# Kernel tuning notes

Measured on AMD Instinct MI355X. Metric: run time of the kernel, lower is better.

Reference implementation:

```python
import jax, jax.numpy as jnp
import numpy as np

B, S, DM = 4, 2048, 512
H, D = 8, 64          # att_head, head_dim = att_dim // att_head
LEFT, RIGHT = 128, 128  # band_part(left_mask, right_mask)
LARGE = 1e30          # masked_softmax large number for fp32


def setup_inputs() -> dict:
    key = jax.random.key(0)
    ks = jax.random.split(key, 11)
    scale = 1.0 / np.sqrt(DM)
    x = jax.random.normal(ks[0], (B, S, DM), jnp.float32)
    Wq = jax.random.normal(ks[1], (DM, DM), jnp.float32) * scale
    bq = jnp.zeros((DM,), jnp.float32)
    Wk = jax.random.normal(ks[2], (DM, DM), jnp.float32) * scale
    bk = jnp.zeros((DM,), jnp.float32)
    Wv = jax.random.normal(ks[3], (DM, DM), jnp.float32) * scale
    bv = jnp.zeros((DM,), jnp.float32)
    Wo = jax.random.normal(ks[4], (DM, DM), jnp.float32) * scale
    bo = jnp.zeros((DM,), jnp.float32)
    x_len = jax.random.randint(ks[5], (B,), 0, 2048)
    return {"x": x, "Wq": Wq, "bq": bq, "Wk": Wk, "bk": bk,
            "Wv": Wv, "bv": bv, "Wo": Wo, "bo": bo, "x_len": x_len}


def reference(x, Wq, bq, Wk, bk, Wv, bv, Wo, bo, x_len):
    b, s, _ = x.shape
    # QKV projections, split into heads: [B,S,H,D]
    q = (x @ Wq + bq).reshape(b, s, H, D)
    k = (x @ Wk + bk).reshape(b, s, H, D)
    v = (x @ Wv + bv).reshape(b, s, H, D)
    # content energy: [B,H,Q,K], scaled by sqrt(head_dim)
    energy = jnp.einsum('bind,bjnd->bnij', q, k) / jnp.sqrt(jnp.float32(D))
    # banded mask (tf.linalg.band_part semantics): keep -LEFT <= j-i <= RIGHT
    i = jnp.arange(s)[:, None]
    j = jnp.arange(s)[None, :]
    band = ((j - i) <= RIGHT) & ((i - j) <= LEFT)            # [S,S]
    # key-length mask (tf.sequence_mask, expanded to [B,1,1,S])
    seq = jnp.arange(s)[None, :] < x_len[:, None]            # [B,S]
    mask = (band[None, None, :, :] & seq[:, None, None, :]).astype(energy.dtype)
    # masked softmax: energy - (1 - mask) * LARGE, softmax over keys
    att = jax.nn.softmax(energy - (1.0 - mask) * LARGE, axis=-1)
    # context: [B,Q,H,D] -> [B,S,H*D]
    ctx = jnp.einsum('bnij,bjnd->bind', att, v).reshape(b, s, H * D)
    # output projection (use_proj=True)
    return ctx @ Wo + bo
```

## Files before the change

### kernel.cpp

```cpp
#include <hip/hip_runtime.h>

#define S_LEN 2048
#define BATCH 4
#define DMODEL 512
#define NHEAD 8
#define HDIM 64
#define ROWS (BATCH * S_LEN)

using short8 = __attribute__((ext_vector_type(8))) short;
using f32x4  = __attribute__((ext_vector_type(4))) float;

__device__ __forceinline__ unsigned short f2bf(float f) {
  unsigned int u = __builtin_bit_cast(unsigned int, f);
  u += 0x7fffu + ((u >> 16) & 1u);
  return (unsigned short)(u >> 16);
}
__device__ __forceinline__ float bf2f(unsigned short h) {
  unsigned int u = ((unsigned int)h) << 16;
  return __builtin_bit_cast(float, u);
}
__device__ __forceinline__ void glds16(const void* g, void* l) {
  __builtin_amdgcn_global_load_lds((const __attribute__((address_space(1))) unsigned*)g,
                                   (__attribute__((address_space(3))) unsigned*)l, 16, 0, 0);
}

__global__ __launch_bounds__(256) void prep_kernel(const float* __restrict__ x,
                                                   const float* __restrict__ Wq,
                                                   const float* __restrict__ Wk,
                                                   const float* __restrict__ Wv,
                                                   const float* __restrict__ Wo,
                                                   unsigned short* __restrict__ xb,
                                                   unsigned short* __restrict__ WqkT,
                                                   unsigned short* __restrict__ WvT,
                                                   unsigned short* __restrict__ WoT) {
  __shared__ float t[32][33];
  const int blk = blockIdx.x, tid = threadIdx.x;
  if (blk < 2048) {
    const int base = (blk * 256 + tid) * 8;
    float4 f0 = *(const float4*)(x + base);
    float4 f1 = *(const float4*)(x + base + 4);
    uint4 o;
    o.x = (unsigned)f2bf(f0.x) | ((unsigned)f2bf(f0.y) << 16);
    o.y = (unsigned)f2bf(f0.z) | ((unsigned)f2bf(f0.w) << 16);
    o.z = (unsigned)f2bf(f1.x) | ((unsigned)f2bf(f1.y) << 16);
    o.w = (unsigned)f2bf(f1.z) | ((unsigned)f2bf(f1.w) << 16);
    *(uint4*)(xb + base) = o;
    return;
  }
  const int tb = blk - 2048;
  const int which = tb >> 8;
  const int tile = tb & 255;
  const float* W = which == 0 ? Wq : which == 1 ? Wk : which == 2 ? Wv : Wo;
  unsigned short* WT = which == 0 ? WqkT : which == 1 ? (WqkT + 512 * 512)
                      : which == 2 ? WvT : WoT;
  const int tx = tid & 31, ty = tid >> 5;
  const int x0 = (tile & 15) * 32, y0 = (tile >> 4) * 32;
#pragma unroll
  for (int r = 0; r < 4; r++)
    t[ty + 8 * r][tx] = W[(size_t)(y0 + ty + 8 * r) * DMODEL + x0 + tx];
  __syncthreads();
#pragma unroll
  for (int r = 0; r < 4; r++)
    WT[(size_t)(x0 + ty + 8 * r) * DMODEL + y0 + tx] = f2bf(t[tx][ty + 8 * r]);
}

__global__ __launch_bounds__(256, 2) void gemm_qkv_kernel(const unsigned short* __restrict__ xb,
                                                          const unsigned short* __restrict__ WqkT,
                                                          const unsigned short* __restrict__ WvT,
                                                          const float* __restrict__ bq,
                                                          const float* __restrict__ bk,
                                                          const float* __restrict__ bv,
                                                          const int* __restrict__ x_len,
                                                          unsigned short* __restrict__ Qb,
                                                          unsigned short* __restrict__ Kb,
                                                          unsigned short* __restrict__ Vt) {
  constexpr int K = DMODEL;
  __shared__ __align__(16) char smem[16384];
  char* As = smem;
  char* Bs = smem + 8192;
  const int bid = blockIdx.x;
  const bool vmode = bid < 256;
  const unsigned short *A, *Bt;
  int m0, n0;
  if (vmode) {
    m0 = (bid & 3) * 128;
    n0 = (bid >> 2) * 128;
    A = WvT; Bt = xb;
  } else {
    const int q = bid - 256;
    m0 = (q >> 3) * 128;
    n0 = (q & 7) * 128;
    A = xb; Bt = WqkT;
    const int xl = x_len[m0 >> 11];
    const int s0 = m0 & 2047;
    if (n0 >= DMODEL) { if (s0 >= xl) return; }
    else if (s0 >= xl + 128) return;
  }
  const int tid = threadIdx.x;
  const int wave = tid >> 6, lane = tid & 63;
  const int wr = wave >> 1, wc = wave & 1;
  const int lm = lane & 15, lq = lane >> 4;
  const int lr = lane >> 2;
  const int lc = (lane & 3) ^ ((lane >> 3) & 3);
  const unsigned short* gA0 = A + (size_t)(m0 + wave * 16 + lr) * K + lc * 8;
  const unsigned short* gA1 = A + (size_t)(m0 + (wave + 4) * 16 + lr) * K + lc * 8;
  const unsigned short* gB0 = Bt + (size_t)(n0 + wave * 16 + lr) * K + lc * 8;
  const unsigned short* gB1 = Bt + (size_t)(n0 + (wave + 4) * 16 + lr) * K + lc * 8;
  char* lA0 = As + wave * 1024 + lane * 16;
  char* lA1 = As + (wave + 4) * 1024 + lane * 16;
  char* lB0 = Bs + wave * 1024 + lane * 16;
  char* lB1 = Bs + (wave + 4) * 1024 + lane * 16;
  const int sw = (lm >> 1) & 3;
  int aoff[4], boff[4];
#pragma unroll
  for (int mi = 0; mi < 4; mi++)
    aoff[mi] = (wr * 64 + mi * 16 + lm) * 64 + (lq ^ sw) * 16;
#pragma unroll
  for (int ni = 0; ni < 4; ni++)
    boff[ni] = (wc * 64 + ni * 16 + lm) * 64 + (lq ^ sw) * 16;

  f32x4 acc[4][4] = {};
  for (int k0 = 0; k0 < K; k0 += 32) {
    __syncthreads();
    glds16(gA0 + k0, lA0);
    glds16(gA1 + k0, lA1);
    glds16(gB0 + k0, lB0);
    glds16(gB1 + k0, lB1);
    __syncthreads();
    short8 af[4], bfr[4];
#pragma unroll
    for (int mi = 0; mi < 4; mi++) af[mi] = *(const short8*)(As + aoff[mi]);
#pragma unroll
    for (int ni = 0; ni < 4; ni++) bfr[ni] = *(const short8*)(Bs + boff[ni]);
#pragma unroll
    for (int mi = 0; mi < 4; mi++)
#pragma unroll
      for (int ni = 0; ni < 4; ni++)
        acc[mi][ni] = __builtin_amdgcn_mfma_f32_16x16x32_bf16(af[mi], bfr[ni], acc[mi][ni], 0, 0, 0);
  }
#pragma unroll
  for (int mi = 0; mi < 4; mi++) {
    const int row0 = m0 + wr * 64 + mi * 16 + lq * 4;
#pragma unroll
    for (int ni = 0; ni < 4; ni++) {
      const int col = n0 + wc * 64 + ni * 16 + lm;
#pragma unroll
      for (int r = 0; r < 4; r++) {
        const int row = row0 + r;
        const float v = acc[mi][ni][r];
        if (vmode) {
          Vt[(size_t)row * ROWS + col] = f2bf(v + bv[row]);
        } else if (col < DMODEL) {
          Qb[(size_t)row * DMODEL + col] = f2bf(v + bq[col]);
        } else {
          Kb[(size_t)row * DMODEL + (col - DMODEL)] = f2bf(v + bk[col - DMODEL]);
        }
      }
    }
  }
}

__global__ __launch_bounds__(256) void vsum_kernel(const unsigned short* __restrict__ Vt,
                                                   float* __restrict__ vs) {
  const int wid = blockIdx.x * 4 + (threadIdx.x >> 6);
  const int lane = threadIdx.x & 63;
  const int b = wid >> 9, n = wid & 511;
  const unsigned short* row = Vt + (size_t)n * ROWS + b * S_LEN;
  float s = 0.f;
#pragma unroll
  for (int it = 0; it < 4; it++) {
    uint4 v = *(const uint4*)(row + it * 512 + lane * 8);
    unsigned int w[4] = {v.x, v.y, v.z, v.w};
#pragma unroll
    for (int e = 0; e < 4; e++) {
      s += bf2f((unsigned short)(w[e] & 0xffffu));
      s += bf2f((unsigned short)(w[e] >> 16));
    }
  }
#pragma unroll
  for (int off = 1; off < 64; off <<= 1) s += __shfl_xor(s, off, 64);
  if (lane == 0) vs[(size_t)b * DMODEL + n] = s;
}

__global__ __launch_bounds__(256) void tailrow_kernel(const float* __restrict__ vsum,
                                                      const unsigned short* __restrict__ WoT,
                                                      const float* __restrict__ bo,
                                                      float* __restrict__ trow) {
  const int b = blockIdx.y;
  const int wave = threadIdx.x >> 6, lane = threadIdx.x & 63;
  const float* vs = vsum + b * DMODEL + lane * 8;
  float vreg[8];
  *(float4*)vreg = *(const float4*)vs;
  *(float4*)(vreg + 4) = *(const float4*)(vs + 4);
#pragma unroll
  for (int ci = 0; ci < 8; ci++) {
    const int c = blockIdx.x * 32 + wave * 8 + ci;
    const uint4 wv = *(const uint4*)(WoT + (size_t)c * DMODEL + lane * 8);
    const unsigned int w[4] = {wv.x, wv.y, wv.z, wv.w};
    float acc = 0.f;
#pragma unroll
    for (int e = 0; e < 4; e++) {
      acc += vreg[2 * e] * bf2f((unsigned short)(w[e] & 0xffffu));
      acc += vreg[2 * e + 1] * bf2f((unsigned short)(w[e] >> 16));
    }
#pragma unroll
    for (int off = 1; off < 64; off <<= 1) acc += __shfl_xor(acc, off, 64);
    if (lane == 0) trow[b * DMODEL + c] = bo[c] + acc * (1.f / 2048.f);
  }
}

__global__ __launch_bounds__(256) void attn_kernel(const unsigned short* __restrict__ Q,
                                                   const unsigned short* __restrict__ K,
                                                   const unsigned short* __restrict__ Vt,
                                                   const int* __restrict__ x_len,
                                                   const float* __restrict__ vsum,
                                                   unsigned short* __restrict__ ctx) {
  __shared__ unsigned short Ks[32][72];
  __shared__ unsigned short Vs[64][40];
  __shared__ unsigned short Ps[4][16][40];
  const int tid = threadIdx.x;
  const int wave = tid >> 6, lane = tid & 63;
  const int lm = lane & 15, lq = lane >> 4;
  const int b = blockIdx.z, h = blockIdx.y;
  const int i0 = blockIdx.x * 64;
  const int q0 = i0 + wave * 16;
  const int xlen = x_len[b];
  const int t0 = min(S_LEN, xlen + 128);
  if ((i0 & ~127) >= t0) return;

  const size_t qoff = (size_t)(b * S_LEN + q0 + lm) * DMODEL + h * HDIM + lq * 8;
  const short8 aq0 = *(const short8*)(Q + qoff);
  const short8 aq1 = *(const short8*)(Q + qoff + 32);

  const int krow = tid >> 3, kchk = (tid & 7) * 8;
  const int vdim = tid >> 2, vchk = (tid & 3) * 8;

  f32x4 oacc[4] = {};
  float lrow[4] = {0.f, 0.f, 0.f, 0.f};

  for (int kt = 0; kt < 10; kt++) {
    const int jt0 = i0 - 128 + kt * 32;
    if (jt0 + 31 < 0 || jt0 >= xlen) continue;
    __syncthreads();
    {
      const int jr = jt0 + krow;
      const int jrc = min(max(jr, 0), S_LEN - 1);
      *(uint4*)&Ks[krow][kchk] =
          *(const uint4*)(K + (size_t)(b * S_LEN + jrc) * DMODEL + h * HDIM + kchk);
      const int jv = jt0 + vchk;
      const int jvc = min(max(jv, 0), S_LEN - 8);
      *(uint4*)&Vs[vdim][vchk] =
          *(const uint4*)(Vt + (size_t)(h * HDIM + vdim) * ROWS + b * S_LEN + jvc);
    }
    __syncthreads();
    if (jt0 + 31 < q0 - 128 || jt0 > q0 + 143) continue;

    f32x4 sv[2];
#pragma unroll
    for (int sub = 0; sub < 2; sub++) {
      const short8 bk0 = *(const short8*)&Ks[sub * 16 + lm][lq * 8];
      const short8 bk1 = *(const short8*)&Ks[sub * 16 + lm][32 + lq * 8];
      f32x4 s = {};
      s = __builtin_amdgcn_mfma_f32_16x16x32_bf16(aq0, bk0, s, 0, 0, 0);
      s = __builtin_amdgcn_mfma_f32_16x16x32_bf16(aq1, bk1, s, 0, 0, 0);
      sv[sub] = s;
    }
    float p[2][4];
#pragma unroll
    for (int sub = 0; sub < 2; sub++) {
      const int j = jt0 + sub * 16 + lm;
      const bool jv = (j >= 0) && (j < xlen);
#pragma unroll
      for (int r = 0; r < 4; r++) {
        const int i = q0 + lq * 4 + r;
        const bool ok = jv && (j - i <= 128) && (i - j <= 128);
        const float pv = ok ? __expf(sv[sub][r] * 0.125f) : 0.f;
        p[sub][r] = pv;
        lrow[r] += pv;
      }
    }
#pragma unroll
    for (int r = 0; r < 4; r++) {
      Ps[wave][lq * 4 + r][lm] = f2bf(p[0][r]);
      Ps[wave][lq * 4 + r][16 + lm] = f2bf(p[1][r]);
    }
    const short8 pf = *(const short8*)&Ps[wave][lm][lq * 8];
#pragma unroll
    for (int dt = 0; dt < 4; dt++) {
      const short8 bv = *(const short8*)&Vs[dt * 16 + lm][lq * 8];
      oacc[dt] = __builtin_amdgcn_mfma_f32_16x16x32_bf16(pf, bv, oacc[dt], 0, 0, 0);
    }
  }
#pragma unroll
  for (int r = 0; r < 4; r++)
#pragma unroll
    for (int off = 1; off < 16; off <<= 1) lrow[r] += __shfl_xor(lrow[r], off, 64);

#pragma unroll
  for (int r = 0; r < 4; r++) {
    const int i = q0 + lq * 4 + r;
    const size_t obase = (size_t)(b * S_LEN + i) * DMODEL + h * HDIM;
    if (lrow[r] > 0.f) {
      const float inv = 1.f / lrow[r];
#pragma unroll
      for (int dt = 0; dt < 4; dt++)
        ctx[obase + dt * 16 + lm] = f2bf(oacc[dt][r] * inv);
    } else {
#pragma unroll
      for (int dt = 0; dt < 4; dt++)
        ctx[obase + dt * 16 + lm] =
            f2bf(vsum[(size_t)b * DMODEL + h * HDIM + dt * 16 + lm] * (1.f / 2048.f));
    }
  }
}

__global__ __launch_bounds__(256, 2) void gemm_out_kernel(const unsigned short* __restrict__ A,
                                                          const unsigned short* __restrict__ Bt,
                                                          const float* __restrict__ bias,
                                                          const int* __restrict__ x_len,
                                                          const float* __restrict__ trow,
                                                          float* __restrict__ out) {
  constexpr int K = DMODEL;
  __shared__ __align__(16) char smem[16384];
  char* As = smem;
  char* Bs = smem + 8192;
  const int tid = threadIdx.x;
  const int m0 = blockIdx.y * 128, n0 = blockIdx.x * 128;
  {
    const int xl = x_len[m0 >> 11];
    if ((m0 & 2047) >= min(S_LEN, xl + 128)) {
      const float4 val = *(const float4*)(trow + (m0 >> 11) * DMODEL + n0 + (tid & 31) * 4);
      float* obase = out + (size_t)m0 * DMODEL + n0 + (tid & 31) * 4;
#pragma unroll
      for (int r = tid >> 5; r < 128; r += 8)
        *(float4*)(obase + (size_t)r * DMODEL) = val;
      return;
    }
  }
  const int wave = tid >> 6, lane = tid & 63;
  const int wr = wave >> 1, wc = wave & 1;
  const int lm = lane & 15, lq = lane >> 4;
  const int lr = lane >> 2;
  const int lc = (lane & 3) ^ ((lane >> 3) & 3);
  const unsigned short* gA0 = A + (size_t)(m0 + wave * 16 + lr) * K + lc * 8;
  const unsigned short* gA1 = A + (size_t)(m0 + (wave + 4) * 16 + lr) * K + lc * 8;
  const unsigned short* gB0 = Bt + (size_t)(n0 + wave * 16 + lr) * K + lc * 8;
  const unsigned short* gB1 = Bt + (size_t)(n0 + (wave + 4) * 16 + lr) * K + lc * 8;
  char* lA0 = As + wave * 1024 + lane * 16;
  char* lA1 = As + (wave + 4) * 1024 + lane * 16;
  char* lB0 = Bs + wave * 1024 + lane * 16;
  char* lB1 = Bs + (wave + 4) * 1024 + lane * 16;
  const int sw = (lm >> 1) & 3;
  int aoff[4], boff[4];
#pragma unroll
  for (int mi = 0; mi < 4; mi++)
    aoff[mi] = (wr * 64 + mi * 16 + lm) * 64 + (lq ^ sw) * 16;
#pragma unroll
  for (int ni = 0; ni < 4; ni++)
    boff[ni] = (wc * 64 + ni * 16 + lm) * 64 + (lq ^ sw) * 16;

  f32x4 acc[4][4] = {};
  for (int k0 = 0; k0 < K; k0 += 32) {
    __syncthreads();
    glds16(gA0 + k0, lA0);
    glds16(gA1 + k0, lA1);
    glds16(gB0 + k0, lB0);
    glds16(gB1 + k0, lB1);
    __syncthreads();
    short8 af[4], bfr[4];
#pragma unroll
    for (int mi = 0; mi < 4; mi++) af[mi] = *(const short8*)(As + aoff[mi]);
#pragma unroll
    for (int ni = 0; ni < 4; ni++) bfr[ni] = *(const short8*)(Bs + boff[ni]);
#pragma unroll
    for (int mi = 0; mi < 4; mi++)
#pragma unroll
      for (int ni = 0; ni < 4; ni++)
        acc[mi][ni] = __builtin_amdgcn_mfma_f32_16x16x32_bf16(af[mi], bfr[ni], acc[mi][ni], 0, 0, 0);
  }
#pragma unroll
  for (int mi = 0; mi < 4; mi++) {
    const int row0 = m0 + wr * 64 + mi * 16 + lq * 4;
#pragma unroll
    for (int ni = 0; ni < 4; ni++) {
      const int col = n0 + wc * 64 + ni * 16 + lm;
#pragma unroll
      for (int r = 0; r < 4; r++)
        out[(size_t)(row0 + r) * DMODEL + col] = acc[mi][ni][r] + bias[col];
    }
  }
}

extern "C" void kernel_launch(void* const* d_in, const int* in_sizes, int n_in,
                              void* d_out, int out_size, void* d_ws, size_t ws_size,
                              hipStream_t stream) {
  (void)in_sizes; (void)n_in; (void)out_size; (void)ws_size;
  const float* x  = (const float*)d_in[0];
  const float* Wq = (const float*)d_in[1];
  const float* bq = (const float*)d_in[2];
  const float* Wk = (const float*)d_in[3];
  const float* bk = (const float*)d_in[4];
  const float* Wv = (const float*)d_in[5];
  const float* bv = (const float*)d_in[6];
  const float* Wo = (const float*)d_in[7];
  const float* bo = (const float*)d_in[8];
  const int* x_len = (const int*)d_in[9];

  char* ws = (char*)d_ws;
  const size_t MB = 1024 * 1024;
  unsigned short* xb   = (unsigned short*)(ws + 0 * MB);
  unsigned short* Qb   = (unsigned short*)(ws + 8 * MB);
  unsigned short* Kb   = (unsigned short*)(ws + 16 * MB);
  unsigned short* Vt   = (unsigned short*)(ws + 24 * MB);
  unsigned short* Cx   = (unsigned short*)(ws + 32 * MB);
  unsigned short* WqkT = (unsigned short*)(ws + 40 * MB);
  unsigned short* WvT  = (unsigned short*)(ws + 41 * MB);
  unsigned short* WoT  = (unsigned short*)(ws + 41 * MB + 512 * 1024);
  float* vsum          = (float*)(ws + 42 * MB);
  float* trow          = (float*)(ws + 42 * MB + 8192);

  prep_kernel<<<3072, 256, 0, stream>>>(x, Wq, Wk, Wv, Wo, xb, WqkT, WvT, WoT);
  gemm_qkv_kernel<<<768, 256, 0, stream>>>(xb, WqkT, WvT, bq, bk, bv, x_len, Qb, Kb, Vt);
  vsum_kernel<<<512, 256, 0, stream>>>(Vt, vsum);
  tailrow_kernel<<<dim3(16, 4), 256, 0, stream>>>(vsum, WoT, bo, trow);
  attn_kernel<<<dim3(32, 8, 4), 256, 0, stream>>>(Qb, Kb, Vt, x_len, vsum, Cx);
  gemm_out_kernel<<<dim3(4, 64), 256, 0, stream>>>(Cx, WoT, bo, x_len, trow, (float*)d_out);
}
```

Baseline: 148.9 us.

## Fuse all stages into one cooperative persistent kernel with grid syncs

Result: slower. 411.7 us (+176.4%).

```diff
diff --git a/kernel.cpp b/kernel.cpp
--- a/kernel.cpp
+++ b/kernel.cpp
@@ -1,4 +1,7 @@
 #include <hip/hip_runtime.h>
+#include <hip/hip_cooperative_groups.h>
+
+namespace cg = cooperative_groups;
 
 #define S_LEN 2048
 #define BATCH 4
@@ -24,88 +27,77 @@
                                    (__attribute__((address_space(3))) unsigned*)l, 16, 0, 0);
 }
 
-__global__ __launch_bounds__(256) void prep_kernel(const float* __restrict__ x,
-                                                   const float* __restrict__ Wq,
-                                                   const float* __restrict__ Wk,
-                                                   const float* __restrict__ Wv,
-                                                   const float* __restrict__ Wo,
-                                                   unsigned short* __restrict__ xb,
-                                                   unsigned short* __restrict__ WqkT,
-                                                   unsigned short* __restrict__ WvT,
-                                                   unsigned short* __restrict__ WoT) {
-  __shared__ float t[32][33];
-  const int blk = blockIdx.x, tid = threadIdx.x;
-  if (blk < 2048) {
-    const int base = (blk * 256 + tid) * 8;
-    float4 f0 = *(const float4*)(x + base);
-    float4 f1 = *(const float4*)(x + base + 4);
+struct MegaArgs {
+  const float *x, *Wq, *bq, *Wk, *bk, *Wv, *bv, *Wo, *bo;
+  const int* x_len;
+  float* out;
+  unsigned short *xb, *Qb, *Kb, *Vt, *WqkT, *WvT, *WoT, *Cx;
+  float *vsum, *trow;
+};
+
+
+__device__ void phase_prep_unit(const MegaArgs& a, int unit, char* smem) {
+  const int tid = threadIdx.x;
+  if (unit < 2048) {
+    const int base = (unit * 256 + tid) * 8;
+    float4 f0 = *(const float4*)(a.x + base);
+    float4 f1 = *(const float4*)(a.x + base + 4);
     uint4 o;
     o.x = (unsigned)f2bf(f0.x) | ((unsigned)f2bf(f0.y) << 16);
     o.y = (unsigned)f2bf(f0.z) | ((unsigned)f2bf(f0.w) << 16);
     o.z = (unsigned)f2bf(f1.x) | ((unsigned)f2bf(f1.y) << 16);
     o.w = (unsigned)f2bf(f1.z) | ((unsigned)f2bf(f1.w) << 16);
-    *(uint4*)(xb + base) = o;
-    return;
-  }
-  const int tb = blk - 2048;
-  const int which = tb >> 8;
-  const int tile = tb & 255;
-  const float* W = which == 0 ? Wq : which == 1 ? Wk : which == 2 ? Wv : Wo;
-  unsigned short* WT = which == 0 ? WqkT : which == 1 ? (WqkT + 512 * 512)
-                      : which == 2 ? WvT : WoT;
-  const int tx = tid & 31, ty = tid >> 5;
-  const int x0 = (tile & 15) * 32, y0 = (tile >> 4) * 32;
-#pragma unroll
-  for (int r = 0; r < 4; r++)
-    t[ty + 8 * r][tx] = W[(size_t)(y0 + ty + 8 * r) * DMODEL + x0 + tx];
-  __syncthreads();
-#pragma unroll
-  for (int r = 0; r < 4; r++)
-    WT[(size_t)(x0 + ty + 8 * r) * DMODEL + y0 + tx] = f2bf(t[tx][ty + 8 * r]);
-}
-
-__global__ __launch_bounds__(256, 2) void gemm_qkv_kernel(const unsigned short* __restrict__ xb,
-                                                          const unsigned short* __restrict__ WqkT,
-                                                          const unsigned short* __restrict__ WvT,
-                                                          const float* __restrict__ bq,
-                                                          const float* __restrict__ bk,
-                                                          const float* __restrict__ bv,
-                                                          const int* __restrict__ x_len,
-                                                          unsigned short* __restrict__ Qb,
-                                                          unsigned short* __restrict__ Kb,
-                                                          unsigned short* __restrict__ Vt) {
-  constexpr int K = DMODEL;
-  __shared__ __align__(16) char smem[16384];
-  char* As = smem;
-  char* Bs = smem + 8192;
-  const int bid = blockIdx.x;
-  const bool vmode = bid < 256;
+    *(uint4*)(a.xb + base) = o;
+  } else {
+    float (*t)[33] = (float(*)[33])smem;
+    const int tb = unit - 2048;
+    const int which = tb >> 8, tile = tb & 255;
+    const float* W = which == 0 ? a.Wq : which == 1 ? a.Wk : which == 2 ? a.Wv : a.Wo;
+    unsigned short* WT = which == 0 ? a.WqkT : which == 1 ? (a.WqkT + 512 * 512)
+                        : which == 2 ? a.WvT : a.WoT;
+    const int tx = tid & 31, ty = tid >> 5;
+    const int x0 = (tile & 15) * 32, y0 = (tile >> 4) * 32;
+    __syncthreads();
+#pragma unroll
+    for (int r = 0; r < 4; r++)
+      t[ty + 8 * r][tx] = W[(size_t)(y0 + ty + 8 * r) * DMODEL + x0 + tx];
+    __syncthreads();
+#pragma unroll
+    for (int r = 0; r < 4; r++)
+      WT[(size_t)(x0 + ty + 8 * r) * DMODEL + y0 + tx] = f2bf(t[tx][ty + 8 * r]);
+  }
+}
+
+__device__ void phase_qkv_unit(const MegaArgs& a, int unit, char* smem) {
+  const int tid = threadIdx.x;
+  const bool vmode = unit < 256;
   const unsigned short *A, *Bt;
   int m0, n0;
   if (vmode) {
-    m0 = (bid & 3) * 128;
-    n0 = (bid >> 2) * 128;
-    A = WvT; Bt = xb;
+    m0 = (unit & 3) * 128;
+    n0 = (unit >> 2) * 128;
+    A = a.WvT; Bt = a.xb;
   } else {
-    const int q = bid - 256;
+    const int q = unit - 256;
     m0 = (q >> 3) * 128;
     n0 = (q & 7) * 128;
-    A = xb; Bt = WqkT;
-    const int xl = x_len[m0 >> 11];
+    A = a.xb; Bt = a.WqkT;
+    const int xl = a.x_len[m0 >> 11];
     const int s0 = m0 & 2047;
     if (n0 >= DMODEL) { if (s0 >= xl) return; }
     else if (s0 >= xl + 128) return;
   }
-  const int tid = threadIdx.x;
+  char* As = smem;
+  char* Bs = smem + 8192;
   const int wave = tid >> 6, lane = tid & 63;
   const int wr = wave >> 1, wc = wave & 1;
   const int lm = lane & 15, lq = lane >> 4;
   const int lr = lane >> 2;
   const int lc = (lane & 3) ^ ((lane >> 3) & 3);
-  const unsigned short* gA0 = A + (size_t)(m0 + wave * 16 + lr) * K + lc * 8;
-  const unsigned short* gA1 = A + (size_t)(m0 + (wave + 4) * 16 + lr) * K + lc * 8;
-  const unsigned short* gB0 = Bt + (size_t)(n0 + wave * 16 + lr) * K + lc * 8;
-  const unsigned short* gB1 = Bt + (size_t)(n0 + (wave + 4) * 16 + lr) * K + lc * 8;
+  const unsigned short* gA0 = A + (size_t)(m0 + wave * 16 + lr) * DMODEL + lc * 8;
+  const unsigned short* gA1 = A + (size_t)(m0 + (wave + 4) * 16 + lr) * DMODEL + lc * 8;
+  const unsigned short* gB0 = Bt + (size_t)(n0 + wave * 16 + lr) * DMODEL + lc * 8;
+  const unsigned short* gB1 = Bt + (size_t)(n0 + (wave + 4) * 16 + lr) * DMODEL + lc * 8;
   char* lA0 = As + wave * 1024 + lane * 16;
   char* lA1 = As + (wave + 4) * 1024 + lane * 16;
   char* lB0 = Bs + wave * 1024 + lane * 16;
@@ -113,14 +105,11 @@
   const int sw = (lm >> 1) & 3;
   int aoff[4], boff[4];
 #pragma unroll
-  for (int mi = 0; mi < 4; mi++)
-    aoff[mi] = (wr * 64 + mi * 16 + lm) * 64 + (lq ^ sw) * 16;
-#pragma unroll
-  for (int ni = 0; ni < 4; ni++)
-    boff[ni] = (wc * 64 + ni * 16 + lm) * 64 + (lq ^ sw) * 16;
-
+  for (int mi = 0; mi < 4; mi++) aoff[mi] = (wr * 64 + mi * 16 + lm) * 64 + (lq ^ sw) * 16;
+#pragma unroll
+  for (int ni = 0; ni < 4; ni++) boff[ni] = (wc * 64 + ni * 16 + lm) * 64 + (lq ^ sw) * 16;
   f32x4 acc[4][4] = {};
-  for (int k0 = 0; k0 < K; k0 += 32) {
+  for (int k0 = 0; k0 < DMODEL; k0 += 32) {
     __syncthreads();
     glds16(gA0 + k0, lA0);
     glds16(gA1 + k0, lA1);
@@ -149,23 +138,21 @@
         const int row = row0 + r;
         const float v = acc[mi][ni][r];
         if (vmode) {
-          Vt[(size_t)row * ROWS + col] = f2bf(v + bv[row]);
+          a.Vt[(size_t)row * ROWS + col] = f2bf(v + a.bv[row]);
         } else if (col < DMODEL) {
-          Qb[(size_t)row * DMODEL + col] = f2bf(v + bq[col]);
+          a.Qb[(size_t)row * DMODEL + col] = f2bf(v + a.bq[col]);
         } else {
-          Kb[(size_t)row * DMODEL + (col - DMODEL)] = f2bf(v + bk[col - DMODEL]);
+          a.Kb[(size_t)row * DMODEL + (col - DMODEL)] = f2bf(v + a.bk[col - DMODEL]);
         }
       }
     }
   }
 }
 
-__global__ __launch_bounds__(256) void vsum_kernel(const unsigned short* __restrict__ Vt,
-                                                   float* __restrict__ vs) {
-  const int wid = blockIdx.x * 4 + (threadIdx.x >> 6);
+__device__ void phase_vsum_unit(const MegaArgs& a, int wid) {
   const int lane = threadIdx.x & 63;
   const int b = wid >> 9, n = wid & 511;
-  const unsigned short* row = Vt + (size_t)n * ROWS + b * S_LEN;
+  const unsigned short* row = a.Vt + (size_t)n * ROWS + b * S_LEN;
   float s = 0.f;
 #pragma unroll
   for (int it = 0; it < 4; it++) {
@@ -179,173 +166,151 @@
   }
 #pragma unroll
   for (int off = 1; off < 64; off <<= 1) s += __shfl_xor(s, off, 64);
-  if (lane == 0) vs[(size_t)b * DMODEL + n] = s;
-}
-
-__global__ __launch_bounds__(256) void tailrow_kernel(const float* __restrict__ vsum,
-                                                      const unsigned short* __restrict__ WoT,
-                                                      const float* __restrict__ bo,
-                                                      float* __restrict__ trow) {
-  const int b = blockIdx.y;
-  const int wave = threadIdx.x >> 6, lane = threadIdx.x & 63;
-  const float* vs = vsum + b * DMODEL + lane * 8;
-  float vreg[8];
-  *(float4*)vreg = *(const float4*)vs;
-  *(float4*)(vreg + 4) = *(const float4*)(vs + 4);
-#pragma unroll
-  for (int ci = 0; ci < 8; ci++) {
-    const int c = blockIdx.x * 32 + wave * 8 + ci;
-    const uint4 wv = *(const uint4*)(WoT + (size_t)c * DMODEL + lane * 8);
-    const unsigned int w[4] = {wv.x, wv.y, wv.z, wv.w};
-    float acc = 0.f;
-#pragma unroll
-    for (int e = 0; e < 4; e++) {
-      acc += vreg[2 * e] * bf2f((unsigned short)(w[e] & 0xffffu));
-      acc += vreg[2 * e + 1] * bf2f((unsigned short)(w[e] >> 16));
-    }
-#pragma unroll
-    for (int off = 1; off < 64; off <<= 1) acc += __shfl_xor(acc, off, 64);
-    if (lane == 0) trow[b * DMODEL + c] = bo[c] + acc * (1.f / 2048.f);
-  }
-}
-
-__global__ __launch_bounds__(256) void attn_kernel(const unsigned short* __restrict__ Q,
-                                                   const unsigned short* __restrict__ K,
-                                                   const unsigned short* __restrict__ Vt,
-                                                   const int* __restrict__ x_len,
-                                                   const float* __restrict__ vsum,
-                                                   unsigned short* __restrict__ ctx) {
-  __shared__ unsigned short Ks[32][72];
-  __shared__ unsigned short Vs[64][40];
-  __shared__ unsigned short Ps[4][16][40];
+  if (lane == 0) a.vsum[(size_t)b * DMODEL + n] = s;
+}
+
+__device__ void phase_attn_unit(const MegaArgs& a, int unit, char* smem) {
   const int tid = threadIdx.x;
-  const int wave = tid >> 6, lane = tid & 63;
-  const int lm = lane & 15, lq = lane >> 4;
-  const int b = blockIdx.z, h = blockIdx.y;
-  const int i0 = blockIdx.x * 64;
-  const int q0 = i0 + wave * 16;
-  const int xlen = x_len[b];
-  const int t0 = min(S_LEN, xlen + 128);
-  if ((i0 & ~127) >= t0) return;
-
-  const size_t qoff = (size_t)(b * S_LEN + q0 + lm) * DMODEL + h * HDIM + lq * 8;
-  const short8 aq0 = *(const short8*)(Q + qoff);
-  const short8 aq1 = *(const short8*)(Q + qoff + 32);
-
-  const int krow = tid >> 3, kchk = (tid & 7) * 8;
-  const int vdim = tid >> 2, vchk = (tid & 3) * 8;
-
-  f32x4 oacc[4] = {};
-  float lrow[4] = {0.f, 0.f, 0.f, 0.f};
-
-  for (int kt = 0; kt < 10; kt++) {
-    const int jt0 = i0 - 128 + kt * 32;
-    if (jt0 + 31 < 0 || jt0 >= xlen) continue;
-    __syncthreads();
-    {
-      const int jr = jt0 + krow;
-      const int jrc = min(max(jr, 0), S_LEN - 1);
-      *(uint4*)&Ks[krow][kchk] =
-          *(const uint4*)(K + (size_t)(b * S_LEN + jrc) * DMODEL + h * HDIM + kchk);
-      const int jv = jt0 + vchk;
-      const int jvc = min(max(jv, 0), S_LEN - 8);
-      *(uint4*)&Vs[vdim][vchk] =
-          *(const uint4*)(Vt + (size_t)(h * HDIM + vdim) * ROWS + b * S_LEN + jvc);
-    }
-    __syncthreads();
-    if (jt0 + 31 < q0 - 128 || jt0 > q0 + 143) continue;
-
-    f32x4 sv[2];
-#pragma unroll
-    for (int sub = 0; sub < 2; sub++) {
-      const short8 bk0 = *(const short8*)&Ks[sub * 16 + lm][lq * 8];
-      const short8 bk1 = *(const short8*)&Ks[sub * 16 + lm][32 + lq * 8];
-      f32x4 s = {};
-      s = __builtin_amdgcn_mfma_f32_16x16x32_bf16(aq0, bk0, s, 0, 0, 0);
-      s = __builtin_amdgcn_mfma_f32_16x16x32_bf16(aq1, bk1, s, 0, 0, 0);
-      sv[sub] = s;
-    }
-    float p[2][4];
-#pragma unroll
-    for (int sub = 0; sub < 2; sub++) {
-      const int j = jt0 + sub * 16 + lm;
-      const bool jv = (j >= 0) && (j < xlen);
+  if (unit < 1024) {
+    const int b = unit >> 8, h = (unit >> 5) & 7;
+    const int i0 = (unit & 31) * 64;
+    const int xlen = a.x_len[b];
+    const int t0 = min(S_LEN, xlen + 128);
+    if ((i0 & ~127) >= t0) return;
+    unsigned short (*Ks)[72] = (unsigned short(*)[72])smem;
+    unsigned short (*Vs)[40] = (unsigned short(*)[40])(smem + 4608);
+    unsigned short (*Ps)[16][40] = (unsigned short(*)[16][40])(smem + 9728);
+    const int wave = tid >> 6, lane = tid & 63;
+    const int lm = lane & 15, lq = lane >> 4;
+    const int q0 = i0 + wave * 16;
+    const size_t qoff = (size_t)(b * S_LEN + q0 + lm) * DMODEL + h * HDIM + lq * 8;
+    const short8 aq0 = *(const short8*)(a.Qb + qoff);
+    const short8 aq1 = *(const short8*)(a.Qb + qoff + 32);
+    const int krow = tid >> 3, kchk = (tid & 7) * 8;
+    const int vdim = tid >> 2, vchk = (tid & 3) * 8;
+    f32x4 oacc[4] = {};
+    float lrow[4] = {0.f, 0.f, 0.f, 0.f};
+    for (int kt = 0; kt < 10; kt++) {
+      const int jt0 = i0 - 128 + kt * 32;
+      if (jt0 + 31 < 0 || jt0 >= xlen) continue;
+      __syncthreads();
+      {
+        const int jr = jt0 + krow;
+        const int jrc = min(max(jr, 0), S_LEN - 1);
+        *(uint4*)&Ks[krow][kchk] =
+            *(const uint4*)(a.Kb + (size_t)(b * S_LEN + jrc) * DMODEL + h * HDIM + kchk);
+        const int jv = jt0 + vchk;
+        const int jvc = min(max(jv, 0), S_LEN - 8);
+        *(uint4*)&Vs[vdim][vchk] =
+            *(const uint4*)(a.Vt + (size_t)(h * HDIM + vdim) * ROWS + b * S_LEN + jvc);
+      }
+      __syncthreads();
+      if (jt0 + 31 < q0 - 128 || jt0 > q0 + 143) continue;
+      f32x4 sv[2];
+#pragma unroll
+      for (int sub = 0; sub < 2; sub++) {
+        const short8 bk0 = *(const short8*)&Ks[sub * 16 + lm][lq * 8];
+        const short8 bk1 = *(const short8*)&Ks[sub * 16 + lm][32 + lq * 8];
+        f32x4 s = {};
+        s = __builtin_amdgcn_mfma_f32_16x16x32_bf16(aq0, bk0, s, 0, 0, 0);
+        s = __builtin_amdgcn_mfma_f32_16x16x32_bf16(aq1, bk1, s, 0, 0, 0);
+        sv[sub] = s;
+      }
+      float p[2][4];
+#pragma unroll
+      for (int sub = 0; sub < 2; sub++) {
+        const int j = jt0 + sub * 16 + lm;
+        const bool jv = (j >= 0) && (j < xlen);
+#pragma unroll
+        for (int r = 0; r < 4; r++) {
+          const int i = q0 + lq * 4 + r;
+          const bool ok = jv && (j - i <= 128) && (i - j <= 128);
+          const float pv = ok ? __expf(sv[sub][r] * 0.125f) : 0.f;
+          p[sub][r] = pv;
+          lrow[r] += pv;
+        }
+      }
 #pragma unroll
       for (int r = 0; r < 4; r++) {
-        const int i = q0 + lq * 4 + r;
-        const bool ok = jv && (j - i <= 128) && (i - j <= 128);
-        const float pv = ok ? __expf(sv[sub][r] * 0.125f) : 0.f;
-        p[sub][r] = pv;
-        lrow[r] += pv;
-      }
-    }
+        Ps[wave][lq * 4 + r][lm] = f2bf(p[0][r]);
+        Ps[wave][lq * 4 + r][16 + lm] = f2bf(p[1][r]);
+      }
+      const short8 pf = *(const short8*)&Ps[wave][lm][lq * 8];
+#pragma unroll
+      for (int dt = 0; dt < 4; dt++) {
+        const short8 bv = *(const short8*)&Vs[dt * 16 + lm][lq * 8];
+        oacc[dt] = __builtin_amdgcn_mfma_f32_16x16x32_bf16(pf, bv, oacc[dt], 0, 0, 0);
+      }
+    }
+#pragma unroll
+    for (int r = 0; r < 4; r++)
+#pragma unroll
+      for (int off = 1; off < 16; off <<= 1) lrow[r] += __shfl_xor(lrow[r], off, 64);
 #pragma unroll
     for (int r = 0; r < 4; r++) {
-      Ps[wave][lq * 4 + r][lm] = f2bf(p[0][r]);
-      Ps[wave][lq * 4 + r][16 + lm] = f2bf(p[1][r]);
-    }
-    const short8 pf = *(const short8*)&Ps[wave][lm][lq * 8];
-#pragma unroll
-    for (int dt = 0; dt < 4; dt++) {
-      const short8 bv = *(const short8*)&Vs[dt * 16 + lm][lq * 8];
-      oacc[dt] = __builtin_amdgcn_mfma_f32_16x16x32_bf16(pf, bv, oacc[dt], 0, 0, 0);
-    }
-  }
-#pragma unroll
-  for (int r = 0; r < 4; r++)
-#pragma unroll
-    for (int off = 1; off < 16; off <<= 1) lrow[r] += __shfl_xor(lrow[r], off, 64);
-
-#pragma unroll
-  for (int r = 0; r < 4; r++) {
-    const int i = q0 + lq * 4 + r;
-    const size_t obase = (size_t)(b * S_LEN + i) * DMODEL + h * HDIM;
-    if (lrow[r] > 0.f) {
-      const float inv = 1.f / lrow[r];
-#pragma unroll
-      for (int dt = 0; dt < 4; dt++)
-        ctx[obase + dt * 16 + lm] = f2bf(oacc[dt][r] * inv);
-    } else {
-#pragma unroll
-      for (int dt = 0; dt < 4; dt++)
-        ctx[obase + dt * 16 + lm] =
-            f2bf(vsum[(size_t)b * DMODEL + h * HDIM + dt * 16 + lm] * (1.f / 2048.f));
-    }
-  }
-}
-
-__global__ __launch_bounds__(256, 2) void gemm_out_kernel(const unsigned short* __restrict__ A,
-                                                          const unsigned short* __restrict__ Bt,
-                                                          const float* __restrict__ bias,
-                                                          const int* __restrict__ x_len,
-                                                          const float* __restrict__ trow,
-                                                          float* __restrict__ out) {
-  constexpr int K = DMODEL;
-  __shared__ __align__(16) char smem[16384];
+      const int i = q0 + lq * 4 + r;
+      const size_t obase = (size_t)(b * S_LEN + i) * DMODEL + h * HDIM;
+      if (lrow[r] > 0.f) {
+        const float inv = 1.f / lrow[r];
+#pragma unroll
+        for (int dt = 0; dt < 4; dt++)
+          a.Cx[obase + dt * 16 + lm] = f2bf(oacc[dt][r] * inv);
+      } else {
+#pragma unroll
+        for (int dt = 0; dt < 4; dt++)
+          a.Cx[obase + dt * 16 + lm] =
+              f2bf(a.vsum[(size_t)b * DMODEL + h * HDIM + dt * 16 + lm] * (1.f / 2048.f));
+      }
+    }
+  } else {
+    const int u = unit - 1024;
+    const int b = u >> 4;
+    const int wave = tid >> 6, lane = tid & 63;
+    const float* vs = a.vsum + b * DMODEL + lane * 8;
+    float vreg[8];
+    *(float4*)vreg = *(const float4*)vs;
+    *(float4*)(vreg + 4) = *(const float4*)(vs + 4);
+#pragma unroll
+    for (int ci = 0; ci < 8; ci++) {
+      const int c = (u & 15) * 32 + wave * 8 + ci;
+      const uint4 wv = *(const uint4*)(a.WoT + (size_t)c * DMODEL + lane * 8);
+      const unsigned int w[4] = {wv.x, wv.y, wv.z, wv.w};
+      float acc = 0.f;
+#pragma unroll
+      for (int e = 0; e < 4; e++) {
+        acc += vreg[2 * e] * bf2f((unsigned short)(w[e] & 0xffffu));
+        acc += vreg[2 * e + 1] * bf2f((unsigned short)(w[e] >> 16));
+      }
+#pragma unroll
+      for (int off = 1; off < 64; off <<= 1) acc += __shfl_xor(acc, off, 64);
+      if (lane == 0) a.trow[b * DMODEL + c] = a.bo[c] + acc * (1.f / 2048.f);
+    }
+  }
+}
+
+__device__ void phase_out_unit(const MegaArgs& a, int unit, char* smem) {
+  const int tid = threadIdx.x;
+  const int m0 = (unit >> 2) * 128, n0 = (unit & 3) * 128;
+  const int xl = a.x_len[m0 >> 11];
+  if ((m0 & 2047) >= min(S_LEN, xl + 128)) {
+    const float4 val = *(const float4*)(a.trow + (m0 >> 11) * DMODEL + n0 + (tid & 31) * 4);
+    float* obase = a.out + (size_t)m0 * DMODEL + n0 + (tid & 31) * 4;
+#pragma unroll
+    for (int r = tid >> 5; r < 128; r += 8)
+      *(float4*)(obase + (size_t)r * DMODEL) = val;
+    return;
+  }
   char* As = smem;
   char* Bs = smem + 8192;
-  const int tid = threadIdx.x;
-  const int m0 = blockIdx.y * 128, n0 = blockIdx.x * 128;
-  {
-    const int xl = x_len[m0 >> 11];
-    if ((m0 & 2047) >= min(S_LEN, xl + 128)) {
-      const float4 val = *(const float4*)(trow + (m0 >> 11) * DMODEL + n0 + (tid & 31) * 4);
-      float* obase = out + (size_t)m0 * DMODEL + n0 + (tid & 31) * 4;
-#pragma unroll
-      for (int r = tid >> 5; r < 128; r += 8)
-        *(float4*)(obase + (size_t)r * DMODEL) = val;
-      return;
-    }
-  }
   const int wave = tid >> 6, lane = tid & 63;
   const int wr = wave >> 1, wc = wave & 1;
   const int lm = lane & 15, lq = lane >> 4;
   const int lr = lane >> 2;
   const int lc = (lane & 3) ^ ((lane >> 3) & 3);
-  const unsigned short* gA0 = A + (size_t)(m0 + wave * 16 + lr) * K + lc * 8;
-  const unsigned short* gA1 = A + (size_t)(m0 + (wave + 4) * 16 + lr) * K + lc * 8;
-  const unsigned short* gB0 = Bt + (size_t)(n0 + wave * 16 + lr) * K + lc * 8;
-  const unsigned short* gB1 = Bt + (size_t)(n0 + (wave + 4) * 16 + lr) * K + lc * 8;
+  const unsigned short* gA0 = a.Cx + (size_t)(m0 + wave * 16 + lr) * DMODEL + lc * 8;
+  const unsigned short* gA1 = a.Cx + (size_t)(m0 + (wave + 4) * 16 + lr) * DMODEL + lc * 8;
+  const unsigned short* gB0 = a.WoT + (size_t)(n0 + wave * 16 + lr) * DMODEL + lc * 8;
+  const unsigned short* gB1 = a.WoT + (size_t)(n0 + (wave + 4) * 16 + lr) * DMODEL + lc * 8;
   char* lA0 = As + wave * 1024 + lane * 16;
   char* lA1 = As + (wave + 4) * 1024 + lane * 16;
   char* lB0 = Bs + wave * 1024 + lane * 16;
@@ -353,14 +318,11 @@
   const int sw = (lm >> 1) & 3;
   int aoff[4], boff[4];
 #pragma unroll
-  for (int mi = 0; mi < 4; mi++)
-    aoff[mi] = (wr * 64 + mi * 16 + lm) * 64 + (lq ^ sw) * 16;
-#pragma unroll
-  for (int ni = 0; ni < 4; ni++)
-    boff[ni] = (wc * 64 + ni * 16 + lm) * 64 + (lq ^ sw) * 16;
-
+  for (int mi = 0; mi < 4; mi++) aoff[mi] = (wr * 64 + mi * 16 + lm) * 64 + (lq ^ sw) * 16;
+#pragma unroll
+  for (int ni = 0; ni < 4; ni++) boff[ni] = (wc * 64 + ni * 16 + lm) * 64 + (lq ^ sw) * 16;
   f32x4 acc[4][4] = {};
-  for (int k0 = 0; k0 < K; k0 += 32) {
+  for (int k0 = 0; k0 < DMODEL; k0 += 32) {
     __syncthreads();
     glds16(gA0 + k0, lA0);
     glds16(gA1 + k0, lA1);
@@ -386,43 +348,95 @@
       const int col = n0 + wc * 64 + ni * 16 + lm;
 #pragma unroll
       for (int r = 0; r < 4; r++)
-        out[(size_t)(row0 + r) * DMODEL + col] = acc[mi][ni][r] + bias[col];
-    }
-  }
+        a.out[(size_t)(row0 + r) * DMODEL + col] = acc[mi][ni][r] + a.bo[col];
+    }
+  }
+}
+
+__global__ __launch_bounds__(256, 2) void mega_kernel(MegaArgs a) {
+  __shared__ __align__(16) char smem[16384];
+  const int nb = gridDim.x;
+  cg::grid_group grid = cg::this_grid();
+  for (int unit = blockIdx.x; unit < 3072; unit += nb) phase_prep_unit(a, unit, smem);
+  __threadfence();
+  grid.sync();
+  for (int unit = blockIdx.x; unit < 768; unit += nb) phase_qkv_unit(a, unit, smem);
+  __threadfence();
+  grid.sync();
+  for (int wid = blockIdx.x * 4 + (threadIdx.x >> 6); wid < 2048; wid += nb * 4)
+    phase_vsum_unit(a, wid);
+  __threadfence();
+  grid.sync();
+  for (int unit = blockIdx.x; unit < 1088; unit += nb) phase_attn_unit(a, unit, smem);
+  __threadfence();
+  grid.sync();
+  for (int unit = blockIdx.x; unit < 256; unit += nb) phase_out_unit(a, unit, smem);
+}
+
+__global__ __launch_bounds__(256, 2) void fb_prep(MegaArgs a) {
+  __shared__ __align__(16) char smem[16384];
+  phase_prep_unit(a, blockIdx.x, smem);
+}
+__global__ __launch_bounds__(256, 2) void fb_qkv(MegaArgs a) {
+  __shared__ __align__(16) char smem[16384];
+  phase_qkv_unit(a, blockIdx.x, smem);
+}
+__global__ __launch_bounds__(256) void fb_vsum(MegaArgs a) {
+  phase_vsum_unit(a, blockIdx.x * 4 + (threadIdx.x >> 6));
+}
+__global__ __launch_bounds__(256) void fb_attn(MegaArgs a) {
+  __shared__ __align__(16) char smem[16384];
+  phase_attn_unit(a, blockIdx.x, smem);
+}
+__global__ __launch_bounds__(256, 2) void fb_out(MegaArgs a) {
+  __shared__ __align__(16) char smem[16384];
+  phase_out_unit(a, blockIdx.x, smem);
 }
 
 extern "C" void kernel_launch(void* const* d_in, const int* in_sizes, int n_in,
                               void* d_out, int out_size, void* d_ws, size_t ws_size,
                               hipStream_t stream) {
   (void)in_sizes; (void)n_in; (void)out_size; (void)ws_size;
-  const float* x  = (const float*)d_in[0];
-  const float* Wq = (const float*)d_in[1];
-  const float* bq = (const float*)d_in[2];
-  const float* Wk = (const float*)d_in[3];
-  const float* bk = (const float*)d_in[4];
-  const float* Wv = (const float*)d_in[5];
-  const float* bv = (const float*)d_in[6];
-  const float* Wo = (const float*)d_in[7];
-  const float* bo = (const float*)d_in[8];
-  const int* x_len = (const int*)d_in[9];
-
   char* ws = (char*)d_ws;
   const size_t MB = 1024 * 1024;
-  unsigned short* xb   = (unsigned short*)(ws + 0 * MB);
-  unsigned short* Qb   = (unsigned short*)(ws + 8 * MB);
-  unsigned short* Kb   = (unsigned short*)(ws + 16 * MB);
-  unsigned short* Vt   = (unsigned short*)(ws + 24 * MB);
-  unsigned short* Cx   = (unsigned short*)(ws + 32 * MB);
-  unsigned short* WqkT = (unsigned short*)(ws + 40 * MB);
-  unsigned short* WvT  = (unsigned short*)(ws + 41 * MB);
-  unsigned short* WoT  = (unsigned short*)(ws + 41 * MB + 512 * 1024);
-  float* vsum          = (float*)(ws + 42 * MB);
-  float* trow          = (float*)(ws + 42 * MB + 8192);
-
-  prep_kernel<<<3072, 256, 0, stream>>>(x, Wq, Wk, Wv, Wo, xb, WqkT, WvT, WoT);
-  gemm_qkv_kernel<<<768, 256, 0, stream>>>(xb, WqkT, WvT, bq, bk, bv, x_len, Qb, Kb, Vt);
-  vsum_kernel<<<512, 256, 0, stream>>>(Vt, vsum);
-  tailrow_kernel<<<dim3(16, 4), 256, 0, stream>>>(vsum, WoT, bo, trow);
-  attn_kernel<<<dim3(32, 8, 4), 256, 0, stream>>>(Qb, Kb, Vt, x_len, vsum, Cx);
-  gemm_out_kernel<<<dim3(4, 64), 256, 0, stream>>>(Cx, WoT, bo, x_len, trow, (float*)d_out);
-}
+  MegaArgs args;
+  args.x  = (const float*)d_in[0];
+  args.Wq = (const float*)d_in[1];
+  args.bq = (const float*)d_in[2];
+  args.Wk = (const float*)d_in[3];
+  args.bk = (const float*)d_in[4];
+  args.Wv = (const float*)d_in[5];
+  args.bv = (const float*)d_in[6];
+  args.Wo = (const float*)d_in[7];
+  args.bo = (const float*)d_in[8];
+  args.x_len = (const int*)d_in[9];
+  args.out = (float*)d_out;
+  args.xb   = (unsigned short*)(ws + 0 * MB);
+  args.Qb   = (unsigned short*)(ws + 8 * MB);
+  args.Kb   = (unsigned short*)(ws + 16 * MB);
+  args.Vt   = (unsigned short*)(ws + 24 * MB);
+  args.Cx   = (unsigned short*)(ws + 32 * MB);
+  args.WqkT = (unsigned short*)(ws + 40 * MB);
+  args.WvT  = (unsigned short*)(ws + 41 * MB);
+  args.WoT  = (unsigned short*)(ws + 41 * MB + 512 * 1024);
+  args.vsum = (float*)(ws + 42 * MB);
+  args.trow = (float*)(ws + 42 * MB + 8192);
+
+  int maxBlk = 0;
+  hipError_t oe = hipOccupancyMaxActiveBlocksPerMultiprocessor(
+      &maxBlk, (const void*)mega_kernel, 256, 0);
+  hipError_t le = hipErrorUnknown;
+  if (oe == hipSuccess && maxBlk >= 1) {
+    const int grid = maxBlk >= 2 ? 512 : 256;
+    void* kargs[] = {&args};
+    le = hipLaunchCooperativeKernel((const void*)mega_kernel, dim3(grid), dim3(256),
+                                    kargs, 0, stream);
+  }
+  if (le != hipSuccess) {
+    fb_prep<<<3072, 256, 0, stream>>>(args);
+    fb_qkv<<<768, 256, 0, stream>>>(args);
+    fb_vsum<<<512, 256, 0, stream>>>(args);
+    fb_attn<<<1088, 256, 0, stream>>>(args);
+    fb_out<<<256, 256, 0, stream>>>(args);
+  }
+}
```
